# Kernel optimization log

Hardware: AMD Instinct MI355X
Metric: run time of the kernel (lower is better)

## Reference

```python
import jax, jax.numpy as jnp
import numpy as np

# ---- hyperparameters matching init_kwargs / input_specs ----
K = 16          # max neighbors kept per node (avg degree)
ALPHA = 0.5     # FGW trade-off (POT default used in the repo)
FW_ITERS = 5    # Frank-Wolfe (conditional-gradient) outer iterations
SK_ITERS = 20   # log-domain Sinkhorn inner iterations
REG = 0.1       # entropic regularization for the inner OT solve
NEG = -1e9      # "log(0)" for masked (padded) neighborhood slots


def build_neighbors(edge_index, n, k):
    """Fixed-size (padded) neighbor table from a COO edge list."""
    src, dst = edge_index[0], edge_index[1]
    order = jnp.argsort(src)
    s_src, s_dst = src[order], dst[order]
    ids = jnp.arange(n)
    start = jnp.searchsorted(s_src, ids)
    end = jnp.searchsorted(s_src, ids, side='right')
    cnt = jnp.minimum(end - start, k)                       # [n]
    pos = start[:, None] + jnp.arange(k)[None, :]           # [n,k]
    valid = jnp.arange(k)[None, :] < cnt[:, None]           # [n,k]
    nbrs = s_dst[jnp.clip(pos, 0, s_src.shape[0] - 1)]      # [n,k]
    return nbrs, valid


def reference(x, edge_index, templates, templates_features):
    n, d = x.shape
    nbrs, valid = build_neighbors(edge_index, n, K)
    # local node set per node: self + up to K neighbors -> K1 = K+1 slots
    S = jnp.concatenate([jnp.arange(n)[:, None], nbrs], axis=1)            # [n,K1]
    mask = jnp.concatenate([jnp.ones((n, 1), bool), valid], axis=1)        # [n,K1]
    mf = mask.astype(x.dtype)

    # local subgraph adjacency: A[i,a,b] = 1 iff edge S[i,a] -> S[i,b]
    nbrs_of = nbrs[S]                                                      # [n,K1,K]
    valid_of = valid[S]
    eq = (nbrs_of[:, :, None, :] == S[:, None, :, None]) & valid_of[:, :, None, :]
    C1 = eq.any(-1).astype(x.dtype) * mf[:, :, None] * mf[:, None, :]      # [n,K1,K1]

    F1 = x[S] * mf[:, :, None]                                             # [n,K1,d]
    F2 = templates_features                                                # [T,t,d]
    # squared-euclidean feature cost M[i,T,a,b] = ||F1[i,a]-F2[T,b]||^2
    M = (jnp.sum(F1 ** 2, -1)[:, None, :, None]
         + jnp.sum(F2 ** 2, -1)[None, :, None, :]
         - 2.0 * jnp.einsum('nad,tbd->ntab', F1, F2))                      # [n,T,K1,t]

    cnt1 = mf.sum(1)                                                       # [n] (>=1: self)
    p = mf / cnt1[:, None]                                                 # [n,K1] uniform masked
    t_n = templates.shape[1]
    q = jnp.full((t_n,), 1.0 / t_n, x.dtype)
    C2 = templates                                                         # [T,t,t]

    # GW square-loss decomposition (POT): tens = constC - 2*C1 @ T @ C2^T
    constC = (jnp.einsum('nab,nb->na', C1 ** 2, p)[:, None, :, None]
              + jnp.einsum('tab,b->ta', C2 ** 2, q)[None, :, None, :])     # [n,T,K1,t]

    def tens_of(T):
        tmp = jnp.einsum('nac,ntcd->ntad', C1, T)
        cross = jnp.einsum('ntad,tbd->ntab', tmp, C2)
        return constC - 2.0 * cross

    logp = jnp.where(mask, -jnp.log(cnt1)[:, None], NEG)[:, None, :]       # [n,1,K1]
    logq = -jnp.log(jnp.asarray(t_n, x.dtype))                             # scalar

    def sinkhorn(G):
        logK = -G / REG                                                    # [n,T,K1,t]
        f = jnp.zeros(G.shape[:3], G.dtype)
        g = jnp.zeros(G.shape[:2] + (t_n,), G.dtype)
        def body(_, fg):
            f, g = fg
            g = logq - jax.nn.logsumexp(logK + f[..., :, None], axis=-2)
            f = logp - jax.nn.logsumexp(logK + g[..., None, :], axis=-1)
            return (f, g)
        f, g = jax.lax.fori_loop(0, SK_ITERS, body, (f, g))
        return jnp.exp(f[..., :, None] + g[..., None, :] + logK)

    T0 = p[:, None, :, None] * q[None, None, None, :]                      # [n,1->T,K1,t]
    T0 = jnp.broadcast_to(T0, M.shape)

    def fw_step(T, k):
        tens = tens_of(T)
        G = (1.0 - ALPHA) * M + 2.0 * ALPHA * tens                         # FGW gradient
        Tn = sinkhorn(G)                                                   # linear-min oracle
        gamma = 2.0 / (k + 2.0)
        return (1.0 - gamma) * T + gamma * Tn, None

    T, _ = jax.lax.scan(fw_step, T0, jnp.arange(FW_ITERS, dtype=x.dtype))

    tens = tens_of(T)
    dist = ((1.0 - ALPHA) * jnp.sum(M * T, axis=(-2, -1))
            + ALPHA * jnp.sum(tens * T, axis=(-2, -1)))                    # [n,T]
    return dist


def setup_inputs() -> dict:
    key = jax.random.key(0)
    k1, k2, k3, k4 = jax.random.split(key, 4)
    n, d, e = 10000, 128, 160000
    n_T, t_n = 10, 10
    x = jax.random.normal(k1, (n, d), jnp.float32)
    edge_index = jax.random.randint(k2, (2, e), 0, n, jnp.int64)
    templates = jax.random.uniform(k3, (n_T, t_n, t_n), jnp.float32)
    templates_features = jax.random.normal(k4, (n_T, t_n, d), jnp.float32)
    return {"x": x, "edge_index": edge_index,
            "templates": templates, "templates_features": templates_features}
```

## Files before the change

kernel.cpp:

```cpp
#include <hip/hip_runtime.h>
#include <math.h>

#define NNODE 10000
#define NEDGE 160000
#define KNB   16
#define K1    17
#define NT    10
#define TN    10
#define DF    128
#define CAP   64
#define NPAIR (NNODE * NT)
#define NEG_BIG (-1e9f)

#define LOGQ2      (-3.32192809489f)
#define KB_SCALE   (-14.4269504089f)
#define CR_SCALE   (28.8539008178f)
#define G_SCALE    (-0.069314718056f)
#define LN2        0.69314718056f
#define TINYF      1e-30f

#if defined(__has_builtin)
#if __has_builtin(__builtin_amdgcn_exp2f)
#define EXP2F(x) __builtin_amdgcn_exp2f(x)
#endif
#if __has_builtin(__builtin_amdgcn_rcpf)
#define RCPF(x) __builtin_amdgcn_rcpf(x)
#endif
#endif
#ifndef EXP2F
#define EXP2F(x) __expf((x) * LN2)
#endif
#ifndef RCPF
#define RCPF(x) (1.0f / (x))
#endif
#define LOG2F(x) __log2f(x)

#define CBAR() asm volatile("" ::: "memory")

typedef float f32x2 __attribute__((ext_vector_type(2)));

__device__ __forceinline__ f32x2 mk2(float x, float y) { f32x2 r; r.x = x; r.y = y; return r; }
__device__ __forceinline__ f32x2 pk_add(f32x2 a, f32x2 b) { return a + b; }
__device__ __forceinline__ f32x2 pk_sub(f32x2 a, f32x2 b) { return a - b; }
__device__ __forceinline__ f32x2 pk_mul(f32x2 a, f32x2 b) { return a * b; }
__device__ __forceinline__ f32x2 pk_fma(f32x2 a, f32x2 b, f32x2 c) {
  return __builtin_elementwise_fma(a, b, c);
}
__device__ __forceinline__ f32x2 pk_max(f32x2 a, f32x2 b) {
  return mk2(fmaxf(a.x, b.x), fmaxf(a.y, b.y));
}
__device__ __forceinline__ f32x2 pk_exp2(f32x2 a) { return mk2(EXP2F(a.x), EXP2F(a.y)); }
__device__ __forceinline__ float clamp120(float x) { return fminf(120.f, fmaxf(-120.f, x)); }

__device__ __forceinline__ int detect_wide_wave(const int* ei) {
  int z = 0;
  if ((threadIdx.x & 63) == 0) {
#pragma unroll
    for (int i = 0; i < 32; ++i) z |= ei[2 * i + 1];
  }
  z = __shfl(z, 0, 64);
  return z == 0;
}

__global__ void __launch_bounds__(256) k_prep(const int* __restrict__ ei,
                                              int* cnt, int* ebuf,
                                              const float* __restrict__ x,
                                              const float* __restrict__ tf,
                                              const float* __restrict__ tmpl,
                                              float* __restrict__ dots,
                                              float* __restrict__ nxv,
                                              float* __restrict__ nF2,
                                              float* __restrict__ Bq) {
  __shared__ float xs[16][DF];
  const int tid = threadIdx.x;
  if (blockIdx.x < 625) {
    int wide = detect_wide_wave(ei);
    int e = blockIdx.x * 256 + tid;
    int s = wide ? ei[2 * e] : ei[e];
    int pos = atomicAdd(&cnt[s], 1);
    if (pos < CAP) ebuf[s * CAP + pos] = e;
    return;
  }
  const int db = blockIdx.x - 625;
  if (db == 0 && tid < NT * TN) {
    const float* fp = tf + (size_t)tid * DF;
    float s = 0.f;
    for (int d = 0; d < DF; ++d) { float v = fp[d]; s += v * v; }
    nF2[tid] = s;
    const float* cp = tmpl + (size_t)tid * TN;
    float s2 = 0.f;
    for (int c = 0; c < TN; ++c) { float v = cp[c]; s2 += v * v; }
    Bq[tid] = 0.1f * s2;
  }
  const int nb = db * 16;
  const int nvalid = (NNODE - nb) < 16 ? (NNODE - nb) : 16;
  {
    const float4* xg = (const float4*)(x + (size_t)nb * DF);
    float4* xl = (float4*)&xs[0][0];
    for (int i = tid; i < nvalid * (DF / 4); i += 256) xl[i] = xg[i];
  }
  __syncthreads();
  for (int o = tid; o < nvalid * (NT * TN); o += 256) {
    int n = o / (NT * TN);
    int tb = o - n * (NT * TN);
    const float4* fp = (const float4*)(tf + (size_t)tb * DF);
    const float4* xp = (const float4*)&xs[n][0];
    float s = 0.f;
#pragma unroll
    for (int d = 0; d < DF / 4; ++d) {
      float4 a = xp[d], f = fp[d];
      s += a.x * f.x + a.y * f.y + a.z * f.z + a.w * f.w;
    }
    dots[(size_t)(nb + n) * (NT * TN) + tb] = s;
  }
  if (tid < nvalid) {
    const float4* xp = (const float4*)&xs[tid][0];
    float s = 0.f;
#pragma unroll
    for (int d = 0; d < DF / 4; ++d) {
      float4 a = xp[d];
      s += a.x * a.x + a.y * a.y + a.z * a.z + a.w * a.w;
    }
    nxv[nb + tid] = s;
  }
}

__global__ void __launch_bounds__(256) k_select(const int* __restrict__ ei,
                                                const int* __restrict__ cnt,
                                                const int* __restrict__ ebuf,
                                                int* __restrict__ nbrs,
                                                int* __restrict__ kcnt,
                                                int* __restrict__ Sg) {
  const int wv = threadIdx.x >> 6;
  const int lane = threadIdx.x & 63;
  const int i = blockIdx.x * 4 + wv;
  if (i >= NNODE) return;
  const int wide = detect_wide_wave(ei);
  int c = cnt[i]; c = c > CAP ? CAP : c;
  int v = (lane < c) ? ebuf[i * CAP + lane] : 0x7FFFFFFF;
#pragma unroll
  for (int k = 2; k <= 64; k <<= 1) {
#pragma unroll
    for (int j = k >> 1; j > 0; j >>= 1) {
      int pv = __shfl_xor(v, j, 64);
      bool up = ((lane & k) == 0);
      bool lower = ((lane & j) == 0);
      int mn = v < pv ? v : pv;
      int mx = v < pv ? pv : v;
      v = (lower == up) ? mn : mx;
    }
  }
  const int m = c < KNB ? c : KNB;
  if (lane == 0) { kcnt[i] = m; Sg[i * K1] = i; }
  if (lane < KNB) {
    int d = 0;
    if (lane < m) d = wide ? ei[2 * (NEDGE + v)] : ei[NEDGE + v];
    nbrs[i * KNB + lane] = d;
    Sg[i * K1 + 1 + lane] = d;
  }
}

__global__ void __launch_bounds__(256) k_c1b(const int* __restrict__ nbrs,
                                             const int* __restrict__ kcnt,
                                             const int* __restrict__ Sg,
                                             unsigned int* __restrict__ bitsG,
                                             float* __restrict__ Ag) {
  int idx = blockIdx.x * 256 + threadIdx.x;
  if (idx >= NNODE * K1) return;
  int i = idx / K1;
  int a = idx - i * K1;
  int kc = kcnt[i];
  unsigned int vmask = (kc >= KNB) ? 0x1FFFFu : ((2u << kc) - 1u);
  unsigned int bits = 0;
  bool va = (a == 0) || (a - 1 < kc);
  if (va) {
    int S[K1];
#pragma unroll
    for (int b = 0; b < K1; ++b) S[b] = Sg[i * K1 + b];
    int u = S[a];
    int ku = kcnt[u];
    const int* np = nbrs + (size_t)u * KNB;
    for (int j = 0; j < ku; ++j) {
      int w = np[j];
#pragma unroll
      for (int b = 0; b < K1; ++b) bits |= (S[b] == w) ? (1u << b) : 0u;
    }
    bits &= vmask;
  }
  bitsG[idx] = bits;
  Ag[idx] = (float)__popc(bits) / (float)(1 + kc);
}

__global__ void __launch_bounds__(128, 3) k_main(
    const float* __restrict__ tmpl,
    const int* __restrict__ kcnt, const int* __restrict__ Sg,
    const unsigned int* __restrict__ bitsG, const float* __restrict__ Ag,
    const float* __restrict__ dots, const float* __restrict__ nxv,
    const float* __restrict__ nF2, const float* __restrict__ Bq,
    float* __restrict__ out)
{
  __shared__ float SH[2 * 7 * 204 + 16];

  const int wv = threadIdx.x >> 6;
  const int lane = threadIdx.x & 63;
  const int p0 = lane / 10;
  const int b = lane - p0 * 10;
  const int pairRaw = blockIdx.x * 12 + wv * 6 + p0;
  const bool act = (p0 < 6) && (pairRaw < NPAIR);
  const int pair = act ? pairRaw : 0;
  const int node = pair / 10;
  const int tI = pair - node * 10;
  const int tb = tI * TN + b;

  float* const KTp  = &SH[(wv * 7 + p0) * 204];
  float* const fLp  = KTp;
  float* const gLp  = KTp + 20;
  float* const uLp  = KTp;
  float* const wLp  = KTp + 20;
  float* const accp = KTp + 32;

  const int kc = kcnt[node];
  const float cnt1 = (float)(1 + kc);
  const float inv_cnt1 = 1.f / cnt1;
  const float logp2v = -LOG2F(cnt1);
  const float lp2_r0 = ((b == 0) || (b - 1 < kc)) ? logp2v : NEG_BIG;
  const float lp2_r1 = ((9 + b) < kc) ? logp2v : NEG_BIG;

  f32x2 c2v[5];
  {
    const f32x2* cp = (const f32x2*)(tmpl + (size_t)tb * TN);
#pragma unroll
    for (int j = 0; j < 5; ++j) c2v[j] = cp[j];
  }
  const float Bb = Bq[tb];
  const float nf2b = nF2[tb];

  f32x2 Kb2v[8]; float kb16;
  f32x2 Tp2[10];
#pragma unroll
  for (int j = 0; j < 10; ++j) Tp2[j] = mk2(0.f, 0.f);
  unsigned int bw[K1];
#pragma unroll
  for (int a = 0; a < K1; ++a) {
    bool va = (a == 0) || (a - 1 < kc);
    int sa = Sg[node * K1 + a];
    float Ma = (va ? (nxv[sa] - 2.f * dots[(size_t)sa * (NT * TN) + tb]) : 0.f) + nf2b;
    float base = 0.5f * Ma + Ag[node * K1 + a] + Bb;
    float kv = KB_SCALE * base;
    float tv = va ? (inv_cnt1 * 0.1f) : 0.f;
    if (a == 16) kb16 = kv;
    else if (a & 1) Kb2v[a >> 1].y = kv;
    else Kb2v[a >> 1].x = kv;
    if (a < 10) Tp2[a].x = tv; else Tp2[a - 10].y = tv;
    bw[a] = bitsG[node * K1 + a];
  }

  f32x2 Kc2v[8]; float k16 = 0.f;
  f32x2 Kr0v[5], Kr1v[5];
  f32x2 gr[5];
  float g2 = 0.f, fr0 = 0.f, fr1 = 0.f;

#pragma unroll 1
  for (int k = 0; k < 6; ++k) {
#pragma unroll
    for (int a = 0; a < K1; ++a)
      KTp[a * 12 + b] = (a < 10) ? Tp2[a].x : Tp2[a - 10].y;
    CBAR();
    float R[K1];
#pragma unroll
    for (int c = 0; c < K1; ++c) {
      const float* row = &KTp[c * 12];
      float4 u0 = *(const float4*)row;
      float4 u1 = *(const float4*)(row + 4);
      f32x2 u2 = *(const f32x2*)(row + 8);
      f32x2 accA = pk_mul(mk2(u0.x, u0.y), c2v[0]);
      accA = pk_fma(mk2(u0.z, u0.w), c2v[1], accA);
      f32x2 accB = pk_mul(mk2(u1.x, u1.y), c2v[2]);
      accB = pk_fma(mk2(u1.z, u1.w), c2v[3], accB);
      accA = pk_fma(u2, c2v[4], accA);
      accA = pk_add(accA, accB);
      R[c] = accA.x + accA.y;
    }
#pragma unroll
    for (int a = 0; a < K1; ++a) {
      float cr = 0.f;
      unsigned int m = bw[a];
      if (m) {
#pragma unroll
        for (int c = 0; c < K1; ++c)
          if (m & (1u << c)) cr += R[c];
      }
      float base = (a == 16) ? kb16 : ((a & 1) ? Kb2v[a >> 1].y : Kb2v[a >> 1].x);
      float val = base + CR_SCALE * cr;
      if (a == 16) k16 = val;
      else if (a & 1) Kc2v[a >> 1].y = val;
      else Kc2v[a >> 1].x = val;
    }

    if (k == 5) {
      float acc = 0.f;
#pragma unroll
      for (int a = 0; a < K1; ++a) {
        bool va = (a == 0) || (a - 1 < kc);
        int sa = Sg[node * K1 + a];
        float Ma = (va ? (nxv[sa] - 2.f * dots[(size_t)sa * (NT * TN) + tb]) : 0.f) + nf2b;
        float kcv = (a == 16) ? k16 : ((a & 1) ? Kc2v[a >> 1].y : Kc2v[a >> 1].x);
        float tpv = (a < 10) ? Tp2[a].x : Tp2[a - 10].y;
        acc += tpv * (0.25f * Ma + 0.5f * (G_SCALE * kcv));
      }
      accp[b] = acc;
      CBAR();
      if (act && b == 0) {
        float s = 0.f;
#pragma unroll
        for (int j = 0; j < TN; ++j) s += accp[j];
        out[node * NT + tI] = s;
      }
      return;
    }

    CBAR();
#pragma unroll
    for (int a = 0; a < 16; ++a) KTp[a * 12 + b] = (a & 1) ? Kc2v[a >> 1].y : Kc2v[a >> 1].x;
    KTp[16 * 12 + b] = k16;
    CBAR();
    {
      const float* r0 = &KTp[b * 12];
      float4 u0 = *(const float4*)r0;
      float4 u1 = *(const float4*)(r0 + 4);
      f32x2 u2 = *(const f32x2*)(r0 + 8);
      Kr0v[0] = mk2(u0.x, u0.y); Kr0v[1] = mk2(u0.z, u0.w);
      Kr0v[2] = mk2(u1.x, u1.y); Kr0v[3] = mk2(u1.z, u1.w);
      Kr0v[4] = u2;
      const float* r1 = &KTp[(10 + b) * 12];
      float4 w0 = *(const float4*)r1;
      float4 w1 = *(const float4*)(r1 + 4);
      f32x2 w2 = *(const f32x2*)(r1 + 8);
      Kr1v[0] = mk2(w0.x, w0.y); Kr1v[1] = mk2(w0.z, w0.w);
      Kr1v[2] = mk2(w1.x, w1.y); Kr1v[3] = mk2(w1.z, w1.w);
      Kr1v[4] = w2;
    }

#pragma unroll 1
    for (int it = 0; it < 2; ++it) {
      f32x2 v[8]; float v16;
      if (it == 0) {
#pragma unroll
        for (int i = 0; i < 8; ++i) v[i] = Kc2v[i];
        v16 = k16;
      } else {
        float4 f0 = *(const float4*)&fLp[0];
        float4 f1 = *(const float4*)&fLp[4];
        float4 f2 = *(const float4*)&fLp[8];
        float4 f3 = *(const float4*)&fLp[12];
        float fx = fLp[16];
        v[0] = pk_add(Kc2v[0], mk2(f0.x, f0.y));
        v[1] = pk_add(Kc2v[1], mk2(f0.z, f0.w));
        v[2] = pk_add(Kc2v[2], mk2(f1.x, f1.y));
        v[3] = pk_add(Kc2v[3], mk2(f1.z, f1.w));
        v[4] = pk_add(Kc2v[4], mk2(f2.x, f2.y));
        v[5] = pk_add(Kc2v[5], mk2(f2.z, f2.w));
        v[6] = pk_add(Kc2v[6], mk2(f3.x, f3.y));
        v[7] = pk_add(Kc2v[7], mk2(f3.z, f3.w));
        v16 = k16 + fx;
      }
      f32x2 m01 = pk_max(pk_max(v[0], v[1]), pk_max(v[2], v[3]));
      f32x2 m23 = pk_max(pk_max(v[4], v[5]), pk_max(v[6], v[7]));
      f32x2 mm = pk_max(m01, m23);
      float mx = fmaxf(fmaxf(mm.x, mm.y), v16);
      f32x2 mxb = mk2(mx, mx);
      f32x2 ssA = pk_exp2(pk_sub(v[0], mxb));
      ssA = pk_add(ssA, pk_exp2(pk_sub(v[1], mxb)));
      ssA = pk_add(ssA, pk_exp2(pk_sub(v[2], mxb)));
      ssA = pk_add(ssA, pk_exp2(pk_sub(v[3], mxb)));
      f32x2 ssB = pk_exp2(pk_sub(v[4], mxb));
      ssB = pk_add(ssB, pk_exp2(pk_sub(v[5], mxb)));
      ssB = pk_add(ssB, pk_exp2(pk_sub(v[6], mxb)));
      ssB = pk_add(ssB, pk_exp2(pk_sub(v[7], mxb)));
      f32x2 ss = pk_add(ssA, ssB);
      float s = ss.x + ss.y + EXP2F(v16 - mx);
      g2 = LOGQ2 - mx - LOG2F(s);
      gLp[b] = g2;
      CBAR();
      {
        float4 g0 = *(const float4*)&gLp[0];
        float4 g1 = *(const float4*)&gLp[4];
        f32x2 gx = *(const f32x2*)&gLp[8];
        gr[0] = mk2(g0.x, g0.y); gr[1] = mk2(g0.z, g0.w);
        gr[2] = mk2(g1.x, g1.y); gr[3] = mk2(g1.z, g1.w);
        gr[4] = gx;
      }
      f32x2 w0[5], w1[5];
#pragma unroll
      for (int j = 0; j < 5; ++j) w0[j] = pk_add(Kr0v[j], gr[j]);
#pragma unroll
      for (int j = 0; j < 5; ++j) w1[j] = pk_add(Kr1v[j], gr[j]);
      f32x2 a01 = pk_max(pk_max(w0[0], w0[1]), pk_max(w0[2], w0[3]));
      a01 = pk_max(a01, w0[4]);
      float mxa = fmaxf(a01.x, a01.y);
      f32x2 b01 = pk_max(pk_max(w1[0], w1[1]), pk_max(w1[2], w1[3]));
      b01 = pk_max(b01, w1[4]);
      float mxb2 = fmaxf(b01.x, b01.y);
      f32x2 mab = mk2(mxa, mxa);
      f32x2 mbb = mk2(mxb2, mxb2);
      f32x2 sx = pk_exp2(pk_sub(w0[0], mab));
      sx = pk_add(sx, pk_exp2(pk_sub(w0[1], mab)));
      sx = pk_add(sx, pk_exp2(pk_sub(w0[2], mab)));
      sx = pk_add(sx, pk_exp2(pk_sub(w0[3], mab)));
      sx = pk_add(sx, pk_exp2(pk_sub(w0[4], mab)));
      f32x2 sy = pk_exp2(pk_sub(w1[0], mbb));
      sy = pk_add(sy, pk_exp2(pk_sub(w1[1], mbb)));
      sy = pk_add(sy, pk_exp2(pk_sub(w1[2], mbb)));
      sy = pk_add(sy, pk_exp2(pk_sub(w1[3], mbb)));
      sy = pk_add(sy, pk_exp2(pk_sub(w1[4], mbb)));
      fr0 = lp2_r0 - mxa - LOG2F(sx.x + sx.y);
      fr1 = lp2_r1 - mxb2 - LOG2F(sy.x + sy.y);
      fLp[b] = fr0;
      fLp[10 + b] = fr1;
      CBAR();
    }

    f32x2 Kcs2[10];
    float P00, P01, Q0;
    f32x2 Krs01[10];
    {
      float4 F0 = *(const float4*)&fLp[0];
      float4 F1 = *(const float4*)&fLp[4];
      float4 F2 = *(const float4*)&fLp[8];
      float4 F3 = *(const float4*)&fLp[12];
      float f16v = fLp[16];
      float fs[K1];
      fs[0] = F0.x; fs[1] = F0.y; fs[2] = F0.z; fs[3] = F0.w;
      fs[4] = F1.x; fs[5] = F1.y; fs[6] = F1.z; fs[7] = F1.w;
      fs[8] = F2.x; fs[9] = F2.y; fs[10] = F2.z; fs[11] = F2.w;
      fs[12] = F3.x; fs[13] = F3.y; fs[14] = F3.z; fs[15] = F3.w;
      fs[16] = f16v;
      float qs[K1];
#pragma unroll
      for (int a = 0; a < K1; ++a) {
        float kcv = (a == 16) ? k16 : ((a & 1) ? Kc2v[a >> 1].y : Kc2v[a >> 1].x);
        qs[a] = kcv + fs[a];
      }
      float sigma = qs[0];
#pragma unroll
      for (int a = 1; a < K1; ++a) sigma = fmaxf(sigma, qs[a]);
#pragma unroll
      for (int j = 0; j < 10; ++j) {
        float kx = EXP2F(qs[j] - sigma);
        float ky = (j < 7) ? EXP2F(qs[10 + j] - sigma) : 0.f;
        Kcs2[j] = mk2(kx, ky);
      }
      Q0 = EXP2F(clamp120(LOGQ2 - sigma - g2));
      f32x2 a0[5], a1[5];
#pragma unroll
      for (int j = 0; j < 5; ++j) a0[j] = pk_add(Kr0v[j], gr[j]);
#pragma unroll
      for (int j = 0; j < 5; ++j) a1[j] = pk_add(Kr1v[j], gr[j]);
      f32x2 r0m = pk_max(pk_max(a0[0], a0[1]), pk_max(a0[2], a0[3]));
      r0m = pk_max(r0m, a0[4]);
      float rho0 = fmaxf(r0m.x, r0m.y);
      f32x2 r1m = pk_max(pk_max(a1[0], a1[1]), pk_max(a1[2], a1[3]));
      r1m = pk_max(r1m, a1[4]);
      float rho1 = fmaxf(r1m.x, r1m.y);
#pragma unroll
      for (int j = 0; j < 5; ++j) {
        Krs01[2 * j]     = mk2(EXP2F(a0[j].x - rho0), EXP2F(a1[j].x - rho1));
        Krs01[2 * j + 1] = mk2(EXP2F(a0[j].y - rho0), EXP2F(a1[j].y - rho1));
      }
      P00 = EXP2F(clamp120((lp2_r0 - rho0) - fr0));
      P01 = (b < 7) ? EXP2F(clamp120((lp2_r1 - rho1) - fr1)) : 0.f;
    }

    float Slast, t0, t1;
    {
      f32x2 SA = pk_add(pk_add(Kcs2[0], Kcs2[1]), pk_add(Kcs2[2], Kcs2[3]));
      f32x2 SB = pk_add(pk_add(Kcs2[4], Kcs2[5]), pk_add(Kcs2[6], Kcs2[7]));
      f32x2 S2 = pk_add(pk_add(SA, SB), pk_add(Kcs2[8], Kcs2[9]));
      float S = fmaxf(S2.x + S2.y, TINYF);
      Slast = S;
      float wb = Q0 * RCPF(S);
      wLp[b] = wb;
      CBAR();
      float4 W0 = *(const float4*)&wLp[0];
      float4 W1 = *(const float4*)&wLp[4];
      f32x2 W2 = *(const f32x2*)&wLp[8];
      f32x2 tA = pk_mul(Krs01[0], mk2(W0.x, W0.x));
      tA = pk_fma(Krs01[1], mk2(W0.y, W0.y), tA);
      tA = pk_fma(Krs01[2], mk2(W0.z, W0.z), tA);
      tA = pk_fma(Krs01[3], mk2(W0.w, W0.w), tA);
      tA = pk_fma(Krs01[4], mk2(W1.x, W1.x), tA);
      f32x2 tB = pk_mul(Krs01[5], mk2(W1.y, W1.y));
      tB = pk_fma(Krs01[6], mk2(W1.z, W1.z), tB);
      tB = pk_fma(Krs01[7], mk2(W1.w, W1.w), tB);
      tB = pk_fma(Krs01[8], mk2(W2.x, W2.x), tB);
      tB = pk_fma(Krs01[9], mk2(W2.y, W2.y), tB);
      f32x2 t01 = pk_add(tA, tB);
      t0 = t01.x; t1 = t01.y;
    }
#pragma unroll 1
    for (int it = 0; it < 17; ++it) {
      float u0 = P00 * RCPF(fmaxf(t0, TINYF));
      float u1 = P01 * RCPF(fmaxf(t1, TINYF));
      *(f32x2*)&uLp[2 * b] = mk2(u0, u1);
      CBAR();
      float4 U0 = *(const float4*)&uLp[0];
      float4 U1 = *(const float4*)&uLp[4];
      float4 U2 = *(const float4*)&uLp[8];
      float4 U3 = *(const float4*)&uLp[12];
      float4 U4 = *(const float4*)&uLp[16];
      f32x2 SA = pk_mul(Kcs2[0], mk2(U0.x, U0.y));
      SA = pk_fma(Kcs2[1], mk2(U0.z, U0.w), SA);
      SA = pk_fma(Kcs2[2], mk2(U1.x, U1.y), SA);
      SA = pk_fma(Kcs2[3], mk2(U1.z, U1.w), SA);
      SA = pk_fma(Kcs2[4], mk2(U2.x, U2.y), SA);
      f32x2 SB = pk_mul(Kcs2[5], mk2(U2.z, U2.w));
      SB = pk_fma(Kcs2[6], mk2(U3.x, U3.y), SB);
      SB = pk_fma(Kcs2[7], mk2(U3.z, U3.w), SB);
      SB = pk_fma(Kcs2[8], mk2(U4.x, U4.y), SB);
      SB = pk_fma(Kcs2[9], mk2(U4.z, U4.w), SB);
      f32x2 S2 = pk_add(SA, SB);
      float S = fmaxf(S2.x + S2.y, TINYF);
      Slast = S;
      float wb = Q0 * RCPF(S);
      wLp[b] = wb;
      CBAR();
      float4 W0 = *(const float4*)&wLp[0];
      float4 W1 = *(const float4*)&wLp[4];
      f32x2 W2 = *(const f32x2*)&wLp[8];
      f32x2 tA = pk_mul(Krs01[0], mk2(W0.x, W0.x));
      tA = pk_fma(Krs01[1], mk2(W0.y, W0.y), tA);
      tA = pk_fma(Krs01[2], mk2(W0.z, W0.z), tA);
      tA = pk_fma(Krs01[3], mk2(W0.w, W0.w), tA);
      tA = pk_fma(Krs01[4], mk2(W1.x, W1.x), tA);
      f32x2 tB = pk_mul(Krs01[5], mk2(W1.y, W1.y));
      tB = pk_fma(Krs01[6], mk2(W1.z, W1.z), tB);
      tB = pk_fma(Krs01[7], mk2(W1.w, W1.w), tB);
      tB = pk_fma(Krs01[8], mk2(W2.x, W2.x), tB);
      tB = pk_fma(Krs01[9], mk2(W2.y, W2.y), tB);
      f32x2 t01 = pk_add(tA, tB);
      t0 = t01.x; t1 = t01.y;
    }

    {
      float u0 = P00 * RCPF(fmaxf(t0, TINYF));
      float u1 = P01 * RCPF(fmaxf(t1, TINYF));
      *(f32x2*)&uLp[2 * b] = mk2(u0, u1);
      CBAR();
      float4 U0 = *(const float4*)&uLp[0];
      float4 U1 = *(const float4*)&uLp[4];
      float4 U2 = *(const float4*)&uLp[8];
      float4 U3 = *(const float4*)&uLp[12];
      float4 U4 = *(const float4*)&uLp[16];
      const float gam = 2.f / ((float)k + 2.f);
      const float gs = gam * 0.1f * RCPF(Slast);
      const float om = 1.f - gam;
      const f32x2 omb = mk2(om, om);
      const f32x2 gsb = mk2(gs, gs);
      f32x2 uu[10];
      uu[0] = mk2(U0.x, U0.y); uu[1] = mk2(U0.z, U0.w);
      uu[2] = mk2(U1.x, U1.y); uu[3] = mk2(U1.z, U1.w);
      uu[4] = mk2(U2.x, U2.y); uu[5] = mk2(U2.z, U2.w);
      uu[6] = mk2(U3.x, U3.y); uu[7] = mk2(U3.z, U3.w);
      uu[8] = mk2(U4.x, U4.y); uu[9] = mk2(U4.z, U4.w);
#pragma unroll
      for (int j = 0; j < 10; ++j)
        Tp2[j] = pk_fma(omb, Tp2[j], pk_mul(gsb, pk_mul(Kcs2[j], uu[j])));
    }
  }
}

extern "C" void kernel_launch(void* const* d_in, const int* in_sizes, int n_in,
                              void* d_out, int out_size, void* d_ws, size_t ws_size,
                              hipStream_t stream) {
  const float* x    = (const float*)d_in[0];
  const int*   ei   = (const int*)d_in[1];
  const float* tmpl = (const float*)d_in[2];
  const float* tf   = (const float*)d_in[3];
  float* out = (float*)d_out;

  int* cnt  = (int*)d_ws;
  int* ebuf = cnt + NNODE;
  int* nbrs = ebuf + (size_t)NNODE * CAP;
  int* kcnt = nbrs + (size_t)NNODE * KNB;
  int* Sg   = kcnt + NNODE;
  unsigned int* bits = (unsigned int*)(Sg + (size_t)NNODE * K1);
  float* Ag   = (float*)(bits + (size_t)NNODE * K1);
  float* dots = Ag + (size_t)NNODE * K1;
  float* nxv  = dots + (size_t)NNODE * (NT * TN);
  float* nF2  = nxv + NNODE;
  float* Bq   = nF2 + NT * TN;

  hipMemsetAsync(cnt, 0, NNODE * sizeof(int), stream);
  k_prep<<<625 + (NNODE + 15) / 16, 256, 0, stream>>>(ei, cnt, ebuf, x, tf, tmpl,
                                                      dots, nxv, nF2, Bq);
  k_select<<<(NNODE + 3) / 4, 256, 0, stream>>>(ei, cnt, ebuf, nbrs, kcnt, Sg);
  k_c1b<<<(NNODE * K1 + 255) / 256, 256, 0, stream>>>(nbrs, kcnt, Sg, bits, Ag);
  k_main<<<(NPAIR + 11) / 12, 128, 0, stream>>>(tmpl, kcnt, Sg, bits, Ag, dots, nxv, nF2, Bq, out);
}
```

Before: 512.3 us.

## Process two (node, template) pairs per 10-lane group in the FGW main kernel

Each 10-lane group now holds the state for two pairs instead of one, with interleaved shared-memory slots (stride 24) so a single vector LDS load serves both pairs. The aim is more independent work per thread to hide LDS and transcendental latency and to halve the barrier and LDS round-trip overhead per pair; the grid halves accordingly. The base-cost terms (Ma, Ag) are now recomputed from global memory each outer iteration instead of kept in registers. The cost is higher register pressure, with launch bounds lowered from 3 to 2 blocks per SIMD, so occupancy may fall.

New measurement: 1.399 ms. 173% more time.

```diff
diff --git a/kernel.cpp b/kernel.cpp
--- a/kernel.cpp
+++ b/kernel.cpp
@@ -38,8 +38,11 @@
 #define CBAR() asm volatile("" ::: "memory")
 
 typedef float f32x2 __attribute__((ext_vector_type(2)));
+typedef float f32x4 __attribute__((ext_vector_type(4)));
 
 __device__ __forceinline__ f32x2 mk2(float x, float y) { f32x2 r; r.x = x; r.y = y; return r; }
+__device__ __forceinline__ f32x2 lo2(f32x4 v) { return __builtin_shufflevector(v, v, 0, 1); }
+__device__ __forceinline__ f32x2 hi2(f32x4 v) { return __builtin_shufflevector(v, v, 2, 3); }
 __device__ __forceinline__ f32x2 pk_add(f32x2 a, f32x2 b) { return a + b; }
 __device__ __forceinline__ f32x2 pk_sub(f32x2 a, f32x2 b) { return a - b; }
 __device__ __forceinline__ f32x2 pk_mul(f32x2 a, f32x2 b) { return a * b; }
@@ -191,7 +194,9 @@
   Ag[idx] = (float)__popc(bits) / (float)(1 + kc);
 }
 
-__global__ void __launch_bounds__(128, 3) k_main(
+#define SLOT_STRIDE 412
+
+__global__ void __launch_bounds__(128, 2) k_main(
     const float* __restrict__ tmpl,
     const int* __restrict__ kcnt, const int* __restrict__ Sg,
     const unsigned int* __restrict__ bitsG, const float* __restrict__ Ag,
@@ -199,236 +204,263 @@
     const float* __restrict__ nF2, const float* __restrict__ Bq,
     float* __restrict__ out)
 {
-  __shared__ float SH[2 * 7 * 204 + 16];
+  __shared__ float SH[2 * 7 * SLOT_STRIDE + 72];
 
   const int wv = threadIdx.x >> 6;
   const int lane = threadIdx.x & 63;
   const int p0 = lane / 10;
   const int b = lane - p0 * 10;
-  const int pairRaw = blockIdx.x * 12 + wv * 6 + p0;
-  const bool act = (p0 < 6) && (pairRaw < NPAIR);
-  const int pair = act ? pairRaw : 0;
-  const int node = pair / 10;
-  const int tI = pair - node * 10;
-  const int tb = tI * TN + b;
-
-  float* const KTp  = &SH[(wv * 7 + p0) * 204];
-  float* const fLp  = KTp;
-  float* const gLp  = KTp + 20;
-  float* const uLp  = KTp;
-  float* const wLp  = KTp + 20;
-  float* const accp = KTp + 32;
-
-  const int kc = kcnt[node];
-  const float cnt1 = (float)(1 + kc);
-  const float inv_cnt1 = 1.f / cnt1;
-  const float logp2v = -LOG2F(cnt1);
-  const float lp2_r0 = ((b == 0) || (b - 1 < kc)) ? logp2v : NEG_BIG;
-  const float lp2_r1 = ((9 + b) < kc) ? logp2v : NEG_BIG;
-
-  f32x2 c2v[5];
-  {
+  const int base2 = (blockIdx.x * 12 + wv * 6 + p0) * 2;
+  const bool act = (p0 < 6) && (base2 < NPAIR);
+
+  float* const KTp = &SH[(wv * 7 + p0) * SLOT_STRIDE];
+
+  int   nodeV[2], tIv[2], tbV[2], kcV[2];
+  float lp_r0[2], lp_r1[2], BbV[2], nf2V[2];
+  f32x2 c2v[2][5];
+  f32x2 Tp2[2][10];
+
+#pragma unroll
+  for (int pp = 0; pp < 2; ++pp) {
+    const int pair = act ? (base2 + pp) : 0;
+    const int node = pair / 10;
+    const int tI = pair - node * 10;
+    const int tb = tI * TN + b;
+    nodeV[pp] = node; tIv[pp] = tI; tbV[pp] = tb;
+    const int kc = kcnt[node];
+    kcV[pp] = kc;
+    const float cnt1 = (float)(1 + kc);
+    const float inv_cnt1 = 1.f / cnt1;
+    const float logp2v = -LOG2F(cnt1);
+    lp_r0[pp] = ((b == 0) || (b - 1 < kc)) ? logp2v : NEG_BIG;
+    lp_r1[pp] = ((9 + b) < kc) ? logp2v : NEG_BIG;
     const f32x2* cp = (const f32x2*)(tmpl + (size_t)tb * TN);
 #pragma unroll
-    for (int j = 0; j < 5; ++j) c2v[j] = cp[j];
-  }
-  const float Bb = Bq[tb];
-  const float nf2b = nF2[tb];
-
-  f32x2 Kb2v[8]; float kb16;
-  f32x2 Tp2[10];
-#pragma unroll
-  for (int j = 0; j < 10; ++j) Tp2[j] = mk2(0.f, 0.f);
-  unsigned int bw[K1];
-#pragma unroll
-  for (int a = 0; a < K1; ++a) {
-    bool va = (a == 0) || (a - 1 < kc);
-    int sa = Sg[node * K1 + a];
-    float Ma = (va ? (nxv[sa] - 2.f * dots[(size_t)sa * (NT * TN) + tb]) : 0.f) + nf2b;
-    float base = 0.5f * Ma + Ag[node * K1 + a] + Bb;
-    float kv = KB_SCALE * base;
-    float tv = va ? (inv_cnt1 * 0.1f) : 0.f;
-    if (a == 16) kb16 = kv;
-    else if (a & 1) Kb2v[a >> 1].y = kv;
-    else Kb2v[a >> 1].x = kv;
-    if (a < 10) Tp2[a].x = tv; else Tp2[a - 10].y = tv;
-    bw[a] = bitsG[node * K1 + a];
-  }
-
-  f32x2 Kc2v[8]; float k16 = 0.f;
-  f32x2 Kr0v[5], Kr1v[5];
-  f32x2 gr[5];
-  float g2 = 0.f, fr0 = 0.f, fr1 = 0.f;
+    for (int j = 0; j < 5; ++j) c2v[pp][j] = cp[j];
+    BbV[pp] = Bq[tb];
+    nf2V[pp] = nF2[tb];
+#pragma unroll
+    for (int j = 0; j < 10; ++j) Tp2[pp][j] = mk2(0.f, 0.f);
+#pragma unroll
+    for (int a = 0; a < K1; ++a) {
+      bool va = (a == 0) || (a - 1 < kc);
+      float tv = va ? (inv_cnt1 * 0.1f) : 0.f;
+      if (a < 10) Tp2[pp][a].x = tv; else Tp2[pp][a - 10].y = tv;
+    }
+  }
 
 #pragma unroll 1
   for (int k = 0; k < 6; ++k) {
-#pragma unroll
-    for (int a = 0; a < K1; ++a)
-      KTp[a * 12 + b] = (a < 10) ? Tp2[a].x : Tp2[a - 10].y;
     CBAR();
-    float R[K1];
-#pragma unroll
-    for (int c = 0; c < K1; ++c) {
-      const float* row = &KTp[c * 12];
-      float4 u0 = *(const float4*)row;
-      float4 u1 = *(const float4*)(row + 4);
-      f32x2 u2 = *(const f32x2*)(row + 8);
-      f32x2 accA = pk_mul(mk2(u0.x, u0.y), c2v[0]);
-      accA = pk_fma(mk2(u0.z, u0.w), c2v[1], accA);
-      f32x2 accB = pk_mul(mk2(u1.x, u1.y), c2v[2]);
-      accB = pk_fma(mk2(u1.z, u1.w), c2v[3], accB);
-      accA = pk_fma(u2, c2v[4], accA);
-      accA = pk_add(accA, accB);
-      R[c] = accA.x + accA.y;
-    }
-#pragma unroll
-    for (int a = 0; a < K1; ++a) {
-      float cr = 0.f;
-      unsigned int m = bw[a];
-      if (m) {
-#pragma unroll
-        for (int c = 0; c < K1; ++c)
-          if (m & (1u << c)) cr += R[c];
-      }
-      float base = (a == 16) ? kb16 : ((a & 1) ? Kb2v[a >> 1].y : Kb2v[a >> 1].x);
-      float val = base + CR_SCALE * cr;
-      if (a == 16) k16 = val;
-      else if (a & 1) Kc2v[a >> 1].y = val;
-      else Kc2v[a >> 1].x = val;
-    }
-
-    if (k == 5) {
-      float acc = 0.f;
+#pragma unroll
+    for (int pp = 0; pp < 2; ++pp) {
+      float* kt = KTp + pp * 12;
+#pragma unroll
+      for (int a = 0; a < K1; ++a)
+        kt[a * 24 + b] = (a < 10) ? Tp2[pp][a].x : Tp2[pp][a - 10].y;
+    }
+    CBAR();
+    float R[2][K1];
+#pragma unroll
+    for (int pp = 0; pp < 2; ++pp) {
+#pragma unroll
+      for (int c = 0; c < K1; ++c) {
+        const float* row = &KTp[c * 24 + pp * 12];
+        f32x4 u0 = *(const f32x4*)row;
+        f32x4 u1 = *(const f32x4*)(row + 4);
+        f32x2 u2 = *(const f32x2*)(row + 8);
+        f32x2 aA = pk_mul(lo2(u0), c2v[pp][0]);
+        aA = pk_fma(hi2(u0), c2v[pp][1], aA);
+        f32x2 aB = pk_mul(lo2(u1), c2v[pp][2]);
+        aB = pk_fma(hi2(u1), c2v[pp][3], aB);
+        aA = pk_fma(u2, c2v[pp][4], aA);
+        aA = pk_add(aA, aB);
+        R[pp][c] = aA.x + aA.y;
+      }
+    }
+    f32x2 Kc2v[2][8]; float k16[2];
+#pragma unroll
+    for (int pp = 0; pp < 2; ++pp) {
+      const int node = nodeV[pp]; const int tb = tbV[pp]; const int kc = kcV[pp];
+      const int* sgp = &Sg[node * K1];
+      const unsigned int* bp = &bitsG[node * K1];
+      const float* agp = &Ag[node * K1];
 #pragma unroll
       for (int a = 0; a < K1; ++a) {
         bool va = (a == 0) || (a - 1 < kc);
-        int sa = Sg[node * K1 + a];
-        float Ma = (va ? (nxv[sa] - 2.f * dots[(size_t)sa * (NT * TN) + tb]) : 0.f) + nf2b;
-        float kcv = (a == 16) ? k16 : ((a & 1) ? Kc2v[a >> 1].y : Kc2v[a >> 1].x);
-        float tpv = (a < 10) ? Tp2[a].x : Tp2[a - 10].y;
-        acc += tpv * (0.25f * Ma + 0.5f * (G_SCALE * kcv));
-      }
-      accp[b] = acc;
+        int sa = sgp[a];
+        float Ma = (va ? (nxv[sa] - 2.f * dots[(size_t)sa * (NT * TN) + tb]) : 0.f) + nf2V[pp];
+        float basev = 0.5f * Ma + agp[a] + BbV[pp];
+        unsigned int m = bp[a];
+        float cr = 0.f;
+        if (m) {
+#pragma unroll
+          for (int c = 0; c < K1; ++c)
+            if (m & (1u << c)) cr += R[pp][c];
+        }
+        float val = KB_SCALE * basev + CR_SCALE * cr;
+        if (a == 16) k16[pp] = val;
+        else if (a & 1) Kc2v[pp][a >> 1].y = val;
+        else Kc2v[pp][a >> 1].x = val;
+      }
+    }
+
+    if (k == 5) {
+#pragma unroll
+      for (int pp = 0; pp < 2; ++pp) {
+        const int node = nodeV[pp]; const int tb = tbV[pp]; const int kc = kcV[pp];
+        const int* sgp = &Sg[node * K1];
+        float acc = 0.f;
+#pragma unroll
+        for (int a = 0; a < K1; ++a) {
+          bool va = (a == 0) || (a - 1 < kc);
+          int sa = sgp[a];
+          float Ma = (va ? (nxv[sa] - 2.f * dots[(size_t)sa * (NT * TN) + tb]) : 0.f) + nf2V[pp];
+          float kcv = (a == 16) ? k16[pp] : ((a & 1) ? Kc2v[pp][a >> 1].y : Kc2v[pp][a >> 1].x);
+          float tpv = (a < 10) ? Tp2[pp][a].x : Tp2[pp][a - 10].y;
+          acc += tpv * (0.25f * Ma + 0.5f * (G_SCALE * kcv));
+        }
+        KTp[128 + 10 * pp + b] = acc;
+      }
       CBAR();
-      if (act && b == 0) {
+      if (act && b < 2) {
+        const float* ap = &KTp[128 + 10 * b];
         float s = 0.f;
 #pragma unroll
-        for (int j = 0; j < TN; ++j) s += accp[j];
-        out[node * NT + tI] = s;
+        for (int j = 0; j < TN; ++j) s += ap[j];
+        int nodeS = b ? nodeV[1] : nodeV[0];
+        int tIS = b ? tIv[1] : tIv[0];
+        out[nodeS * NT + tIS] = s;
       }
       return;
     }
 
     CBAR();
 #pragma unroll
-    for (int a = 0; a < 16; ++a) KTp[a * 12 + b] = (a & 1) ? Kc2v[a >> 1].y : Kc2v[a >> 1].x;
-    KTp[16 * 12 + b] = k16;
+    for (int pp = 0; pp < 2; ++pp) {
+      float* kt = KTp + pp * 12;
+#pragma unroll
+      for (int a = 0; a < 16; ++a) kt[a * 24 + b] = (a & 1) ? Kc2v[pp][a >> 1].y : Kc2v[pp][a >> 1].x;
+      kt[16 * 24 + b] = k16[pp];
+    }
     CBAR();
-    {
-      const float* r0 = &KTp[b * 12];
-      float4 u0 = *(const float4*)r0;
-      float4 u1 = *(const float4*)(r0 + 4);
+    f32x2 Kr0v[2][5], Kr1v[2][5];
+#pragma unroll
+    for (int pp = 0; pp < 2; ++pp) {
+      const float* r0 = &KTp[b * 24 + pp * 12];
+      f32x4 u0 = *(const f32x4*)r0;
+      f32x4 u1 = *(const f32x4*)(r0 + 4);
       f32x2 u2 = *(const f32x2*)(r0 + 8);
-      Kr0v[0] = mk2(u0.x, u0.y); Kr0v[1] = mk2(u0.z, u0.w);
-      Kr0v[2] = mk2(u1.x, u1.y); Kr0v[3] = mk2(u1.z, u1.w);
-      Kr0v[4] = u2;
-      const float* r1 = &KTp[(10 + b) * 12];
-      float4 w0 = *(const float4*)r1;
-      float4 w1 = *(const float4*)(r1 + 4);
+      Kr0v[pp][0] = lo2(u0); Kr0v[pp][1] = hi2(u0);
+      Kr0v[pp][2] = lo2(u1); Kr0v[pp][3] = hi2(u1);
+      Kr0v[pp][4] = u2;
+      const float* r1 = &KTp[(10 + b) * 24 + pp * 12];
+      f32x4 w0 = *(const f32x4*)r1;
+      f32x4 w1 = *(const f32x4*)(r1 + 4);
       f32x2 w2 = *(const f32x2*)(r1 + 8);
-      Kr1v[0] = mk2(w0.x, w0.y); Kr1v[1] = mk2(w0.z, w0.w);
-      Kr1v[2] = mk2(w1.x, w1.y); Kr1v[3] = mk2(w1.z, w1.w);
-      Kr1v[4] = w2;
-    }
-
+      Kr1v[pp][0] = lo2(w0); Kr1v[pp][1] = hi2(w0);
+      Kr1v[pp][2] = lo2(w1); Kr1v[pp][3] = hi2(w1);
+      Kr1v[pp][4] = w2;
+    }
+
+    f32x2 gr[2][5];
+    float g2v[2], fr0v[2], fr1v[2];
 #pragma unroll 1
     for (int it = 0; it < 2; ++it) {
-      f32x2 v[8]; float v16;
-      if (it == 0) {
-#pragma unroll
-        for (int i = 0; i < 8; ++i) v[i] = Kc2v[i];
-        v16 = k16;
-      } else {
-        float4 f0 = *(const float4*)&fLp[0];
-        float4 f1 = *(const float4*)&fLp[4];
-        float4 f2 = *(const float4*)&fLp[8];
-        float4 f3 = *(const float4*)&fLp[12];
-        float fx = fLp[16];
-        v[0] = pk_add(Kc2v[0], mk2(f0.x, f0.y));
-        v[1] = pk_add(Kc2v[1], mk2(f0.z, f0.w));
-        v[2] = pk_add(Kc2v[2], mk2(f1.x, f1.y));
-        v[3] = pk_add(Kc2v[3], mk2(f1.z, f1.w));
-        v[4] = pk_add(Kc2v[4], mk2(f2.x, f2.y));
-        v[5] = pk_add(Kc2v[5], mk2(f2.z, f2.w));
-        v[6] = pk_add(Kc2v[6], mk2(f3.x, f3.y));
-        v[7] = pk_add(Kc2v[7], mk2(f3.z, f3.w));
-        v16 = k16 + fx;
-      }
-      f32x2 m01 = pk_max(pk_max(v[0], v[1]), pk_max(v[2], v[3]));
-      f32x2 m23 = pk_max(pk_max(v[4], v[5]), pk_max(v[6], v[7]));
-      f32x2 mm = pk_max(m01, m23);
-      float mx = fmaxf(fmaxf(mm.x, mm.y), v16);
-      f32x2 mxb = mk2(mx, mx);
-      f32x2 ssA = pk_exp2(pk_sub(v[0], mxb));
-      ssA = pk_add(ssA, pk_exp2(pk_sub(v[1], mxb)));
-      ssA = pk_add(ssA, pk_exp2(pk_sub(v[2], mxb)));
-      ssA = pk_add(ssA, pk_exp2(pk_sub(v[3], mxb)));
-      f32x2 ssB = pk_exp2(pk_sub(v[4], mxb));
-      ssB = pk_add(ssB, pk_exp2(pk_sub(v[5], mxb)));
-      ssB = pk_add(ssB, pk_exp2(pk_sub(v[6], mxb)));
-      ssB = pk_add(ssB, pk_exp2(pk_sub(v[7], mxb)));
-      f32x2 ss = pk_add(ssA, ssB);
-      float s = ss.x + ss.y + EXP2F(v16 - mx);
-      g2 = LOGQ2 - mx - LOG2F(s);
-      gLp[b] = g2;
+#pragma unroll
+      for (int pp = 0; pp < 2; ++pp) {
+        f32x2 v[8]; float v16;
+        if (it == 0) {
+#pragma unroll
+          for (int i = 0; i < 8; ++i) v[i] = Kc2v[pp][i];
+          v16 = k16[pp];
+        } else {
+          const float* fb = &KTp[88 + pp * 20];
+          f32x4 f0 = *(const f32x4*)fb;
+          f32x4 f1 = *(const f32x4*)(fb + 4);
+          f32x4 f2 = *(const f32x4*)(fb + 8);
+          f32x4 f3 = *(const f32x4*)(fb + 12);
+          float fx = fb[16];
+          v[0] = pk_add(Kc2v[pp][0], lo2(f0));
+          v[1] = pk_add(Kc2v[pp][1], hi2(f0));
+          v[2] = pk_add(Kc2v[pp][2], lo2(f1));
+          v[3] = pk_add(Kc2v[pp][3], hi2(f1));
+          v[4] = pk_add(Kc2v[pp][4], lo2(f2));
+          v[5] = pk_add(Kc2v[pp][5], hi2(f2));
+          v[6] = pk_add(Kc2v[pp][6], lo2(f3));
+          v[7] = pk_add(Kc2v[pp][7], hi2(f3));
+          v16 = k16[pp] + fx;
+        }
+        f32x2 m01 = pk_max(pk_max(v[0], v[1]), pk_max(v[2], v[3]));
+        f32x2 m23 = pk_max(pk_max(v[4], v[5]), pk_max(v[6], v[7]));
+        f32x2 mm = pk_max(m01, m23);
+        float mx = fmaxf(fmaxf(mm.x, mm.y), v16);
+        f32x2 mxb = mk2(mx, mx);
+        f32x2 ssA = pk_exp2(pk_sub(v[0], mxb));
+        ssA = pk_add(ssA, pk_exp2(pk_sub(v[1], mxb)));
+        ssA = pk_add(ssA, pk_exp2(pk_sub(v[2], mxb)));
+        ssA = pk_add(ssA, pk_exp2(pk_sub(v[3], mxb)));
+        f32x2 ssB = pk_exp2(pk_sub(v[4], mxb));
+        ssB = pk_add(ssB, pk_exp2(pk_sub(v[5], mxb)));
+        ssB = pk_add(ssB, pk_exp2(pk_sub(v[6], mxb)));
+        ssB = pk_add(ssB, pk_exp2(pk_sub(v[7], mxb)));
+        f32x2 ss = pk_add(ssA, ssB);
+        float s = ss.x + ss.y + EXP2F(v16 - mx);
+        g2v[pp] = LOGQ2 - mx - LOG2F(s);
+        KTp[44 + pp * 12 + b] = g2v[pp];
+      }
       CBAR();
-      {
-        float4 g0 = *(const float4*)&gLp[0];
-        float4 g1 = *(const float4*)&gLp[4];
-        f32x2 gx = *(const f32x2*)&gLp[8];
-        gr[0] = mk2(g0.x, g0.y); gr[1] = mk2(g0.z, g0.w);
-        gr[2] = mk2(g1.x, g1.y); gr[3] = mk2(g1.z, g1.w);
-        gr[4] = gx;
-      }
-      f32x2 w0[5], w1[5];
-#pragma unroll
-      for (int j = 0; j < 5; ++j) w0[j] = pk_add(Kr0v[j], gr[j]);
-#pragma unroll
-      for (int j = 0; j < 5; ++j) w1[j] = pk_add(Kr1v[j], gr[j]);
-      f32x2 a01 = pk_max(pk_max(w0[0], w0[1]), pk_max(w0[2], w0[3]));
-      a01 = pk_max(a01, w0[4]);
-      float mxa = fmaxf(a01.x, a01.y);
-      f32x2 b01 = pk_max(pk_max(w1[0], w1[1]), pk_max(w1[2], w1[3]));
-      b01 = pk_max(b01, w1[4]);
-      float mxb2 = fmaxf(b01.x, b01.y);
-      f32x2 mab = mk2(mxa, mxa);
-      f32x2 mbb = mk2(mxb2, mxb2);
-      f32x2 sx = pk_exp2(pk_sub(w0[0], mab));
-      sx = pk_add(sx, pk_exp2(pk_sub(w0[1], mab)));
-      sx = pk_add(sx, pk_exp2(pk_sub(w0[2], mab)));
-      sx = pk_add(sx, pk_exp2(pk_sub(w0[3], mab)));
-      sx = pk_add(sx, pk_exp2(pk_sub(w0[4], mab)));
-      f32x2 sy = pk_exp2(pk_sub(w1[0], mbb));
-      sy = pk_add(sy, pk_exp2(pk_sub(w1[1], mbb)));
-      sy = pk_add(sy, pk_exp2(pk_sub(w1[2], mbb)));
-      sy = pk_add(sy, pk_exp2(pk_sub(w1[3], mbb)));
-      sy = pk_add(sy, pk_exp2(pk_sub(w1[4], mbb)));
-      fr0 = lp2_r0 - mxa - LOG2F(sx.x + sx.y);
-      fr1 = lp2_r1 - mxb2 - LOG2F(sy.x + sy.y);
-      fLp[b] = fr0;
-      fLp[10 + b] = fr1;
+#pragma unroll
+      for (int pp = 0; pp < 2; ++pp) {
+        const float* gb = &KTp[44 + pp * 12];
+        f32x4 g0 = *(const f32x4*)gb;
+        f32x4 g1 = *(const f32x4*)(gb + 4);
+        f32x2 gx = *(const f32x2*)(gb + 8);
+        gr[pp][0] = lo2(g0); gr[pp][1] = hi2(g0);
+        gr[pp][2] = lo2(g1); gr[pp][3] = hi2(g1);
+        gr[pp][4] = gx;
+        f32x2 w0[5], w1[5];
+#pragma unroll
+        for (int j = 0; j < 5; ++j) w0[j] = pk_add(Kr0v[pp][j], gr[pp][j]);
+#pragma unroll
+        for (int j = 0; j < 5; ++j) w1[j] = pk_add(Kr1v[pp][j], gr[pp][j]);
+        f32x2 a01 = pk_max(pk_max(w0[0], w0[1]), pk_max(w0[2], w0[3]));
+        a01 = pk_max(a01, w0[4]);
+        float mxa = fmaxf(a01.x, a01.y);
+        f32x2 b01 = pk_max(pk_max(w1[0], w1[1]), pk_max(w1[2], w1[3]));
+        b01 = pk_max(b01, w1[4]);
+        float mxb2 = fmaxf(b01.x, b01.y);
+        f32x2 mab = mk2(mxa, mxa);
+        f32x2 mbb = mk2(mxb2, mxb2);
+        f32x2 sx = pk_exp2(pk_sub(w0[0], mab));
+        sx = pk_add(sx, pk_exp2(pk_sub(w0[1], mab)));
+        sx = pk_add(sx, pk_exp2(pk_sub(w0[2], mab)));
+        sx = pk_add(sx, pk_exp2(pk_sub(w0[3], mab)));
+        sx = pk_add(sx, pk_exp2(pk_sub(w0[4], mab)));
+        f32x2 sy = pk_exp2(pk_sub(w1[0], mbb));
+        sy = pk_add(sy, pk_exp2(pk_sub(w1[1], mbb)));
+        sy = pk_add(sy, pk_exp2(pk_sub(w1[2], mbb)));
+        sy = pk_add(sy, pk_exp2(pk_sub(w1[3], mbb)));
+        sy = pk_add(sy, pk_exp2(pk_sub(w1[4], mbb)));
+        fr0v[pp] = lp_r0[pp] - mxa - LOG2F(sx.x + sx.y);
+        fr1v[pp] = lp_r1[pp] - mxb2 - LOG2F(sy.x + sy.y);
+        KTp[88 + pp * 20 + b] = fr0v[pp];
+        KTp[88 + pp * 20 + 10 + b] = fr1v[pp];
+      }
       CBAR();
     }
 
-    f32x2 Kcs2[10];
-    float P00, P01, Q0;
-    f32x2 Krs01[10];
-    {
-      float4 F0 = *(const float4*)&fLp[0];
-      float4 F1 = *(const float4*)&fLp[4];
-      float4 F2 = *(const float4*)&fLp[8];
-      float4 F3 = *(const float4*)&fLp[12];
-      float f16v = fLp[16];
+    f32x2 Kcs2[2][10];
+    f32x2 Krs01[2][10];
+    float P00[2], P01[2], Q0[2];
+#pragma unroll
+    for (int pp = 0; pp < 2; ++pp) {
+      const float* fb = &KTp[88 + pp * 20];
+      f32x4 F0 = *(const f32x4*)fb;
+      f32x4 F1 = *(const f32x4*)(fb + 4);
+      f32x4 F2 = *(const f32x4*)(fb + 8);
+      f32x4 F3 = *(const f32x4*)(fb + 12);
+      float f16v = fb[16];
       float fs[K1];
       fs[0] = F0.x; fs[1] = F0.y; fs[2] = F0.z; fs[3] = F0.w;
       fs[4] = F1.x; fs[5] = F1.y; fs[6] = F1.z; fs[7] = F1.w;
@@ -438,7 +470,7 @@
       float qs[K1];
 #pragma unroll
       for (int a = 0; a < K1; ++a) {
-        float kcv = (a == 16) ? k16 : ((a & 1) ? Kc2v[a >> 1].y : Kc2v[a >> 1].x);
+        float kcv = (a == 16) ? k16[pp] : ((a & 1) ? Kc2v[pp][a >> 1].y : Kc2v[pp][a >> 1].x);
         qs[a] = kcv + fs[a];
       }
       float sigma = qs[0];
@@ -448,14 +480,14 @@
       for (int j = 0; j < 10; ++j) {
         float kx = EXP2F(qs[j] - sigma);
         float ky = (j < 7) ? EXP2F(qs[10 + j] - sigma) : 0.f;
-        Kcs2[j] = mk2(kx, ky);
-      }
-      Q0 = EXP2F(clamp120(LOGQ2 - sigma - g2));
+        Kcs2[pp][j] = mk2(kx, ky);
+      }
+      Q0[pp] = EXP2F(clamp120(LOGQ2 - sigma - g2v[pp]));
       f32x2 a0[5], a1[5];
 #pragma unroll
-      for (int j = 0; j < 5; ++j) a0[j] = pk_add(Kr0v[j], gr[j]);
-#pragma unroll
-      for (int j = 0; j < 5; ++j) a1[j] = pk_add(Kr1v[j], gr[j]);
+      for (int j = 0; j < 5; ++j) a0[j] = pk_add(Kr0v[pp][j], gr[pp][j]);
+#pragma unroll
+      for (int j = 0; j < 5; ++j) a1[j] = pk_add(Kr1v[pp][j], gr[pp][j]);
       f32x2 r0m = pk_max(pk_max(a0[0], a0[1]), pk_max(a0[2], a0[3]));
       r0m = pk_max(r0m, a0[4]);
       float rho0 = fmaxf(r0m.x, r0m.y);
@@ -464,107 +496,125 @@
       float rho1 = fmaxf(r1m.x, r1m.y);
 #pragma unroll
       for (int j = 0; j < 5; ++j) {
-        Krs01[2 * j]     = mk2(EXP2F(a0[j].x - rho0), EXP2F(a1[j].x - rho1));
-        Krs01[2 * j + 1] = mk2(EXP2F(a0[j].y - rho0), EXP2F(a1[j].y - rho1));
-      }
-      P00 = EXP2F(clamp120((lp2_r0 - rho0) - fr0));
-      P01 = (b < 7) ? EXP2F(clamp120((lp2_r1 - rho1) - fr1)) : 0.f;
-    }
-
-    float Slast, t0, t1;
+        Krs01[pp][2 * j]     = mk2(EXP2F(a0[j].x - rho0), EXP2F(a1[j].x - rho1));
+        Krs01[pp][2 * j + 1] = mk2(EXP2F(a0[j].y - rho0), EXP2F(a1[j].y - rho1));
+      }
+      P00[pp] = EXP2F(clamp120((lp_r0[pp] - rho0) - fr0v[pp]));
+      P01[pp] = (b < 7) ? EXP2F(clamp120((lp_r1[pp] - rho1) - fr1v[pp])) : 0.f;
+    }
+
+    float Slast[2], t0v[2], t1v[2];
     {
-      f32x2 SA = pk_add(pk_add(Kcs2[0], Kcs2[1]), pk_add(Kcs2[2], Kcs2[3]));
-      f32x2 SB = pk_add(pk_add(Kcs2[4], Kcs2[5]), pk_add(Kcs2[6], Kcs2[7]));
-      f32x2 S2 = pk_add(pk_add(SA, SB), pk_add(Kcs2[8], Kcs2[9]));
-      float S = fmaxf(S2.x + S2.y, TINYF);
-      Slast = S;
-      float wb = Q0 * RCPF(S);
-      wLp[b] = wb;
+      float wb2[2];
+#pragma unroll
+      for (int pp = 0; pp < 2; ++pp) {
+        f32x2 SA = pk_add(pk_add(Kcs2[pp][0], Kcs2[pp][1]), pk_add(Kcs2[pp][2], Kcs2[pp][3]));
+        f32x2 SB = pk_add(pk_add(Kcs2[pp][4], Kcs2[pp][5]), pk_add(Kcs2[pp][6], Kcs2[pp][7]));
+        f32x2 S2 = pk_add(pk_add(SA, SB), pk_add(Kcs2[pp][8], Kcs2[pp][9]));
+        float S = fmaxf(S2.x + S2.y, TINYF);
+        Slast[pp] = S;
+        wb2[pp] = Q0[pp] * RCPF(S);
+      }
+      *(f32x2*)&KTp[68 + 2 * b] = mk2(wb2[0], wb2[1]);
       CBAR();
-      float4 W0 = *(const float4*)&wLp[0];
-      float4 W1 = *(const float4*)&wLp[4];
-      f32x2 W2 = *(const f32x2*)&wLp[8];
-      f32x2 tA = pk_mul(Krs01[0], mk2(W0.x, W0.x));
-      tA = pk_fma(Krs01[1], mk2(W0.y, W0.y), tA);
-      tA = pk_fma(Krs01[2], mk2(W0.z, W0.z), tA);
-      tA = pk_fma(Krs01[3], mk2(W0.w, W0.w), tA);
-      tA = pk_fma(Krs01[4], mk2(W1.x, W1.x), tA);
-      f32x2 tB = pk_mul(Krs01[5], mk2(W1.y, W1.y));
-      tB = pk_fma(Krs01[6], mk2(W1.z, W1.z), tB);
-      tB = pk_fma(Krs01[7], mk2(W1.w, W1.w), tB);
-      tB = pk_fma(Krs01[8], mk2(W2.x, W2.x), tB);
-      tB = pk_fma(Krs01[9], mk2(W2.y, W2.y), tB);
-      f32x2 t01 = pk_add(tA, tB);
-      t0 = t01.x; t1 = t01.y;
+      f32x4 Wq[5];
+#pragma unroll
+      for (int i = 0; i < 5; ++i) Wq[i] = *(const f32x4*)&KTp[68 + 4 * i];
+#pragma unroll
+      for (int pp = 0; pp < 2; ++pp) {
+        float w0 = pp ? Wq[0].y : Wq[0].x, w1 = pp ? Wq[0].w : Wq[0].z;
+        float w2 = pp ? Wq[1].y : Wq[1].x, w3 = pp ? Wq[1].w : Wq[1].z;
+        float w4 = pp ? Wq[2].y : Wq[2].x, w5 = pp ? Wq[2].w : Wq[2].z;
+        float w6 = pp ? Wq[3].y : Wq[3].x, w7 = pp ? Wq[3].w : Wq[3].z;
+        float w8 = pp ? Wq[4].y : Wq[4].x, w9 = pp ? Wq[4].w : Wq[4].z;
+        f32x2 tA = pk_mul(Krs01[pp][0], mk2(w0, w0));
+        tA = pk_fma(Krs01[pp][1], mk2(w1, w1), tA);
+        tA = pk_fma(Krs01[pp][2], mk2(w2, w2), tA);
+        tA = pk_fma(Krs01[pp][3], mk2(w3, w3), tA);
+        tA = pk_fma(Krs01[pp][4], mk2(w4, w4), tA);
+        f32x2 tB = pk_mul(Krs01[pp][5], mk2(w5, w5));
+        tB = pk_fma(Krs01[pp][6], mk2(w6, w6), tB);
+        tB = pk_fma(Krs01[pp][7], mk2(w7, w7), tB);
+        tB = pk_fma(Krs01[pp][8], mk2(w8, w8), tB);
+        tB = pk_fma(Krs01[pp][9], mk2(w9, w9), tB);
+        f32x2 t01 = pk_add(tA, tB);
+        t0v[pp] = t01.x; t1v[pp] = t01.y;
+      }
     }
 #pragma unroll 1
     for (int it = 0; it < 17; ++it) {
-      float u0 = P00 * RCPF(fmaxf(t0, TINYF));
-      float u1 = P01 * RCPF(fmaxf(t1, TINYF));
-      *(f32x2*)&uLp[2 * b] = mk2(u0, u1);
+      float u0A = P00[0] * RCPF(fmaxf(t0v[0], TINYF));
+      float u1A = P01[0] * RCPF(fmaxf(t1v[0], TINYF));
+      float u0B = P00[1] * RCPF(fmaxf(t0v[1], TINYF));
+      float u1B = P01[1] * RCPF(fmaxf(t1v[1], TINYF));
+      f32x4 uw; uw.x = u0A; uw.y = u1A; uw.z = u0B; uw.w = u1B;
+      *(f32x4*)&KTp[4 * b] = uw;
       CBAR();
-      float4 U0 = *(const float4*)&uLp[0];
-      float4 U1 = *(const float4*)&uLp[4];
-      float4 U2 = *(const float4*)&uLp[8];
-      float4 U3 = *(const float4*)&uLp[12];
-      float4 U4 = *(const float4*)&uLp[16];
-      f32x2 SA = pk_mul(Kcs2[0], mk2(U0.x, U0.y));
-      SA = pk_fma(Kcs2[1], mk2(U0.z, U0.w), SA);
-      SA = pk_fma(Kcs2[2], mk2(U1.x, U1.y), SA);
-      SA = pk_fma(Kcs2[3], mk2(U1.z, U1.w), SA);
-      SA = pk_fma(Kcs2[4], mk2(U2.x, U2.y), SA);
-      f32x2 SB = pk_mul(Kcs2[5], mk2(U2.z, U2.w));
-      SB = pk_fma(Kcs2[6], mk2(U3.x, U3.y), SB);
-      SB = pk_fma(Kcs2[7], mk2(U3.z, U3.w), SB);
-      SB = pk_fma(Kcs2[8], mk2(U4.x, U4.y), SB);
-      SB = pk_fma(Kcs2[9], mk2(U4.z, U4.w), SB);
-      f32x2 S2 = pk_add(SA, SB);
-      float S = fmaxf(S2.x + S2.y, TINYF);
-      Slast = S;
-      float wb = Q0 * RCPF(S);
-      wLp[b] = wb;
+      f32x2 SA0 = mk2(0.f, 0.f), SB0 = mk2(0.f, 0.f);
+      f32x2 SA1 = mk2(0.f, 0.f), SB1 = mk2(0.f, 0.f);
+#pragma unroll
+      for (int j = 0; j < 10; ++j) {
+        f32x4 U = *(const f32x4*)&KTp[4 * j];
+        if (j < 5) { SA0 = pk_fma(Kcs2[0][j], lo2(U), SA0); SA1 = pk_fma(Kcs2[1][j], hi2(U), SA1); }
+        else       { SB0 = pk_fma(Kcs2[0][j], lo2(U), SB0); SB1 = pk_fma(Kcs2[1][j], hi2(U), SB1); }
+      }
+      float wb2[2];
+      {
+        f32x2 S20 = pk_add(SA0, SB0);
+        float S0 = fmaxf(S20.x + S20.y, TINYF);
+        Slast[0] = S0; wb2[0] = Q0[0] * RCPF(S0);
+        f32x2 S21 = pk_add(SA1, SB1);
+        float S1 = fmaxf(S21.x + S21.y, TINYF);
+        Slast[1] = S1; wb2[1] = Q0[1] * RCPF(S1);
+      }
+      *(f32x2*)&KTp[68 + 2 * b] = mk2(wb2[0], wb2[1]);
       CBAR();
-      float4 W0 = *(const float4*)&wLp[0];
-      float4 W1 = *(const float4*)&wLp[4];
-      f32x2 W2 = *(const f32x2*)&wLp[8];
-      f32x2 tA = pk_mul(Krs01[0], mk2(W0.x, W0.x));
-      tA = pk_fma(Krs01[1], mk2(W0.y, W0.y), tA);
-      tA = pk_fma(Krs01[2], mk2(W0.z, W0.z), tA);
-      tA = pk_fma(Krs01[3], mk2(W0.w, W0.w), tA);
-      tA = pk_fma(Krs01[4], mk2(W1.x, W1.x), tA);
-      f32x2 tB = pk_mul(Krs01[5], mk2(W1.y, W1.y));
-      tB = pk_fma(Krs01[6], mk2(W1.z, W1.z), tB);
-      tB = pk_fma(Krs01[7], mk2(W1.w, W1.w), tB);
-      tB = pk_fma(Krs01[8], mk2(W2.x, W2.x), tB);
-      tB = pk_fma(Krs01[9], mk2(W2.y, W2.y), tB);
-      f32x2 t01 = pk_add(tA, tB);
-      t0 = t01.x; t1 = t01.y;
+      f32x4 Wq[5];
+#pragma unroll
+      for (int i = 0; i < 5; ++i) Wq[i] = *(const f32x4*)&KTp[68 + 4 * i];
+#pragma unroll
+      for (int pp = 0; pp < 2; ++pp) {
+        float w0 = pp ? Wq[0].y : Wq[0].x, w1 = pp ? Wq[0].w : Wq[0].z;
+        float w2 = pp ? Wq[1].y : Wq[1].x, w3 = pp ? Wq[1].w : Wq[1].z;
+        float w4 = pp ? Wq[2].y : Wq[2].x, w5 = pp ? Wq[2].w : Wq[2].z;
+        float w6 = pp ? Wq[3].y : Wq[3].x, w7 = pp ? Wq[3].w : Wq[3].z;
+        float w8 = pp ? Wq[4].y : Wq[4].x, w9 = pp ? Wq[4].w : Wq[4].z;
+        f32x2 tA = pk_mul(Krs01[pp][0], mk2(w0, w0));
+        tA = pk_fma(Krs01[pp][1], mk2(w1, w1), tA);
+        tA = pk_fma(Krs01[pp][2], mk2(w2, w2), tA);
+        tA = pk_fma(Krs01[pp][3], mk2(w3, w3), tA);
+        tA = pk_fma(Krs01[pp][4], mk2(w4, w4), tA);
+        f32x2 tB = pk_mul(Krs01[pp][5], mk2(w5, w5));
+        tB = pk_fma(Krs01[pp][6], mk2(w6, w6), tB);
+        tB = pk_fma(Krs01[pp][7], mk2(w7, w7), tB);
+        tB = pk_fma(Krs01[pp][8], mk2(w8, w8), tB);
+        tB = pk_fma(Krs01[pp][9], mk2(w9, w9), tB);
+        f32x2 t01 = pk_add(tA, tB);
+        t0v[pp] = t01.x; t1v[pp] = t01.y;
+      }
     }
 
     {
-      float u0 = P00 * RCPF(fmaxf(t0, TINYF));
-      float u1 = P01 * RCPF(fmaxf(t1, TINYF));
-      *(f32x2*)&uLp[2 * b] = mk2(u0, u1);
+      float u0A = P00[0] * RCPF(fmaxf(t0v[0], TINYF));
+      float u1A = P01[0] * RCPF(fmaxf(t1v[0], TINYF));
+      float u0B = P00[1] * RCPF(fmaxf(t0v[1], TINYF));
+      float u1B = P01[1] * RCPF(fmaxf(t1v[1], TINYF));
+      f32x4 uw; uw.x = u0A; uw.y = u1A; uw.z = u0B; uw.w = u1B;
+      *(f32x4*)&KTp[4 * b] = uw;
       CBAR();
-      float4 U0 = *(const float4*)&uLp[0];
-      float4 U1 = *(const float4*)&uLp[4];
-      float4 U2 = *(const float4*)&uLp[8];
-      float4 U3 = *(const float4*)&uLp[12];
-      float4 U4 = *(const float4*)&uLp[16];
       const float gam = 2.f / ((float)k + 2.f);
-      const float gs = gam * 0.1f * RCPF(Slast);
       const float om = 1.f - gam;
       const f32x2 omb = mk2(om, om);
-      const f32x2 gsb = mk2(gs, gs);
-      f32x2 uu[10];
-      uu[0] = mk2(U0.x, U0.y); uu[1] = mk2(U0.z, U0.w);
-      uu[2] = mk2(U1.x, U1.y); uu[3] = mk2(U1.z, U1.w);
-      uu[4] = mk2(U2.x, U2.y); uu[5] = mk2(U2.z, U2.w);
-      uu[6] = mk2(U3.x, U3.y); uu[7] = mk2(U3.z, U3.w);
-      uu[8] = mk2(U4.x, U4.y); uu[9] = mk2(U4.z, U4.w);
-#pragma unroll
-      for (int j = 0; j < 10; ++j)
-        Tp2[j] = pk_fma(omb, Tp2[j], pk_mul(gsb, pk_mul(Kcs2[j], uu[j])));
+      const float gs0 = gam * 0.1f * RCPF(Slast[0]);
+      const float gs1 = gam * 0.1f * RCPF(Slast[1]);
+      const f32x2 gsb0 = mk2(gs0, gs0);
+      const f32x2 gsb1 = mk2(gs1, gs1);
+#pragma unroll
+      for (int j = 0; j < 10; ++j) {
+        f32x4 U = *(const f32x4*)&KTp[4 * j];
+        Tp2[0][j] = pk_fma(omb, Tp2[0][j], pk_mul(gsb0, pk_mul(Kcs2[0][j], lo2(U))));
+        Tp2[1][j] = pk_fma(omb, Tp2[1][j], pk_mul(gsb1, pk_mul(Kcs2[1][j], hi2(U))));
+      }
     }
   }
 }
@@ -595,5 +645,5 @@
                                                       dots, nxv, nF2, Bq);
   k_select<<<(NNODE + 3) / 4, 256, 0, stream>>>(ei, cnt, ebuf, nbrs, kcnt, Sg);
   k_c1b<<<(NNODE * K1 + 255) / 256, 256, 0, stream>>>(nbrs, kcnt, Sg, bits, Ag);
-  k_main<<<(NPAIR + 11) / 12, 128, 0, stream>>>(tmpl, kcnt, Sg, bits, Ag, dots, nxv, nF2, Bq, out);
-}
+  k_main<<<(NPAIR + 23) / 24, 128, 0, stream>>>(tmpl, kcnt, Sg, bits, Ag, dots, nxv, nF2, Bq, out);
+}
```
